# Optimization experiments

Measured on AMD Instinct MI355X. Metric: run time of the kernel, lower is better.

Reference implementation:

```python
import jax, jax.numpy as jnp
import numpy as np

B, T, HW = 2, 16, 224
S = 14            # patch size after stem: 56 // 4
FEAT = 64 * S * S # 12544 per stream


def _stem(x, w):
    # I3D truncated at MaxPool3d_2a_3x3: Conv3d 7x7x7 stride 2 (+ReLU) then MaxPool (1,3,3) stride (1,2,2)
    y = jax.lax.conv_general_dilated(x, w, window_strides=(2, 2, 2), padding='SAME',
                                     dimension_numbers=('NCDHW', 'OIDHW', 'NCDHW'))
    y = jax.nn.relu(y)
    y = jax.lax.reduce_window(y, -jnp.inf, jax.lax.max,
                              (1, 1, 1, 3, 3), (1, 1, 1, 2, 2), 'SAME')
    return y  # [B,64,8,56,56]


def _fold_and_flatten(x):
    # torch: x.unfold(3,s,s).unfold(4,s,s).permute(0,2,3,4,1,5,6).flatten(4)
    b, c, t, h, w = x.shape
    x = x.reshape(b, c, t, h // S, S, w // S, S)          # (B,C,T,hb,hi,wb,wi)
    x = x.transpose(0, 2, 3, 5, 1, 4, 6)                  # (B,T,hb,wb,C,hi,wi)
    return x.reshape(b, t, h // S, w // S, c * S * S)      # (B,8,4,4,12544)


def _fcl(fr, ff, W1, b1, W2, b2, W3, b3):
    # vectorized over (B,T,H,W); dropout inactive (eval)
    x = jnp.concatenate([fr, ff], axis=-1)                 # (B,8,4,4,25088)
    x = jax.nn.relu(jnp.einsum('bthwf,fk->bthwk', x, W1) + b1)
    x = jax.nn.relu(jnp.einsum('bthwf,fk->bthwk', x, W2) + b2)
    return jax.nn.sigmoid(jnp.einsum('bthwf,fk->bthwk', x, W3) + b3)  # (B,8,4,4,1)


def _get_mask(rgbs, flows, w_rgb, w_flow, W1, b1, W2, b2, W3, b3):
    fr = _fold_and_flatten(_stem(rgbs, w_rgb))
    ff = _fold_and_flatten(_stem(flows, w_flow))
    m = _fcl(fr, ff, W1, b1, W2, b2, W3, b3)[..., 0]       # (B,T=8,H=4,W=4)
    m = jax.image.resize(m[:, None], (m.shape[0], 1, T, HW, HW), method='trilinear')
    return m[:, 0]                                          # (B,16,224,224)


def _masking(rgbs, mask, bg):
    # rgbs*mask + bg*(1-mask), broadcast over channel dim
    return rgbs * mask[:, None] + bg[None, :, None] * (1.0 - mask[:, None])


def _feature_head(x, w_feat, Wl, bl):
    # stand-in for full frozen I3D feature backbone: stem + global pool + linear logits
    y = _stem(x, w_feat)                                    # (B,64,8,56,56)
    pooled = y.mean(axis=(2, 3, 4))                         # (B,64)
    return pooled @ Wl + bl                                 # (B,400)


def setup_inputs() -> dict:
    key = jax.random.key(0)
    ks = jax.random.split(key, 10)
    n = lambda k, s, sc=1.0: jax.random.normal(k, s, dtype=jnp.float32) * sc
    return {
        'rgbs': n(ks[0], (B, 3, T, HW, HW)),
        'flows': n(ks[1], (B, 2, T, HW, HW)),
        'img_background': n(ks[2], (3, HW, HW)),
        'w_rgb': n(ks[3], (64, 3, 7, 7, 7), 0.05),
        'w_flow': n(ks[4], (64, 2, 7, 7, 7), 0.05),
        'w_feat': n(ks[5], (64, 3, 7, 7, 7), 0.05),
        'W1': n(ks[6], (2 * FEAT, 1024), 0.01), 'b1': jnp.zeros((1024,), jnp.float32),
        'W2': n(ks[7], (1024, 256), 0.03), 'b2': jnp.zeros((256,), jnp.float32),
        'W3': n(ks[8], (256, 1), 0.06), 'b3': jnp.zeros((1,), jnp.float32),
        'Wl': n(ks[9], (64, 400), 0.1), 'bl': jnp.zeros((400,), jnp.float32),
    }


def reference(rgbs, flows, img_background, w_rgb, w_flow, w_feat,
              W1, b1, W2, b2, W3, b3, Wl, bl):
    mask = _get_mask(rgbs, flows, w_rgb, w_flow, W1, b1, W2, b2, W3, b3)
    masked0 = _masking(rgbs, mask, img_background)
    masked1 = _masking(rgbs, 1.0 - mask, img_background)
    out0 = _feature_head(masked0, w_feat, Wl, bl)
    out1 = _feature_head(masked1, w_feat, Wl, bl)
    return out0, out1, mask
```

## Files before the change

### kernel.cpp

```cpp
#include <hip/hip_runtime.h>
#include <hip/hip_bf16.h>
#include <math.h>

#define IHW 224
#define DIN 16
#define DOUT 8
#define HO 112
#define PO 56
#define DP 21
#define HP 232
#define WP 240
#define PLANE (HP * WP)

typedef __bf16 bf16x8 __attribute__((ext_vector_type(8)));
typedef float f32x4 __attribute__((ext_vector_type(4)));
typedef float f32x16 __attribute__((ext_vector_type(16)));
typedef ushort u16x8 __attribute__((ext_vector_type(8)));

__device__ __forceinline__ ushort f2bf(float f) {
  uint u = __float_as_uint(f);
  uint r = (u + 0x7FFFu + ((u >> 16) & 1u)) >> 16;
  return (ushort)r;
}
__device__ __forceinline__ float bf2f(ushort u) {
  return __uint_as_float(((uint)u) << 16);
}

__global__ void cvt_pad(const float* __restrict__ in, ushort* __restrict__ out, int nbc) {
  const int v = blockIdx.x * 256 + threadIdx.x;
  const int total = nbc * DP * HP * (WP / 2);
  if (v >= total) return;
  const int pw2 = v % (WP / 2);
  int rest = v / (WP / 2);
  const int pih = rest % HP; rest /= HP;
  const int pid = rest % DP;
  const int bc = rest / DP;
  const int id = pid - 2, ih = pih - 2;
  ushort2 o = make_ushort2(0, 0);
  if (id >= 0 && id < DIN && ih >= 0 && ih < IHW) {
    const float* src = in + ((size_t)(bc * DIN + id) * IHW + ih) * IHW;
    const int iw0 = pw2 * 2 - 2;
    if (iw0 >= 0 && iw0 < IHW) o.x = f2bf(src[iw0]);
    if (iw0 + 1 >= 0 && iw0 + 1 < IHW) o.y = f2bf(src[iw0 + 1]);
  }
  reinterpret_cast<ushort2*>(out)[v] = o;
}

__global__ void masking_pad(const float* __restrict__ rgbs, const float* __restrict__ mask,
                            const float* __restrict__ bg, ushort* __restrict__ out) {
  const int v = blockIdx.x * 256 + threadIdx.x;
  const int total = 12 * DP * HP * (WP / 2);
  if (v >= total) return;
  const int pw2 = v % (WP / 2);
  int rest = v / (WP / 2);
  const int pih = rest % HP; rest /= HP;
  const int pid = rest % DP;
  const int bc = rest / DP;
  const int head = bc / 6;
  const int r6 = bc - head * 6;
  const int b = r6 / 3, c = r6 - (r6 / 3) * 3;
  const int t = pid - 2, ih = pih - 2;
  ushort2 o = make_ushort2(0, 0);
  if (t >= 0 && t < DIN && ih >= 0 && ih < IHW) {
    const float* mrow = mask + ((size_t)(b * DIN + t)) * (IHW * IHW) + ih * IHW;
    const float* rrow = rgbs + ((size_t)((b * 3 + c) * DIN + t)) * (IHW * IHW) + ih * IHW;
    const float* brow = bg + (size_t)c * (IHW * IHW) + ih * IHW;
    const int iw0 = pw2 * 2 - 2;
#pragma unroll
    for (int j = 0; j < 2; j++) {
      const int iw = iw0 + j;
      if (iw >= 0 && iw < IHW) {
        float m = mrow[iw];
        if (head) m = 1.f - m;
        const float val = rrow[iw] * m + brow[iw] * (1.f - m);
        if (j == 0) o.x = f2bf(val); else o.y = f2bf(val);
      }
    }
  }
  reinterpret_cast<ushort2*>(out)[v] = o;
}

template<int C>
__global__ __launch_bounds__(256) void wprep(const float* __restrict__ w, ushort* __restrict__ wB) {
  constexpr int C7 = C * 7, KREAL = C * 49, KPAD = (C == 3) ? 160 : 128;
  const int idx = blockIdx.x * 256 + threadIdx.x;
  if (idx >= 64 * 7 * KPAD) return;
  const int k = idx % KPAD;
  const int rest = idx / KPAD;
  const int kw = rest % 7;
  const int oc = rest / 7;
  float val = 0.f;
  if (k < KREAL) {
    const int kd = k / C7, rem = k % C7, c = rem / 7, kh = rem % 7;
    val = w[(((oc * C + c) * 7 + kd) * 7 + kh) * 7 + kw];
  }
  wB[idx] = f2bf(val);
}

template<int C>
__global__ __launch_bounds__(256, 4) void conv_mfma(
    const ushort* __restrict__ in, const ushort* __restrict__ wB,
    ushort* __restrict__ out)
{
  constexpr int C7 = C * 7, KREAL = C * 49;
  constexpr int KPAD = (C == 3) ? 160 : 128;
  constexpr int NKS = KPAD / 16;
  constexpr int ROWB = KPAD * 2;
  constexpr int KG = KPAD / 4;
  constexpr int SROWS = 118;
  constexpr int NU2 = KG * 64 / 256;
  constexpr int BAT = NU2 / 2;

  __shared__ char smem[SROWS * ROWB];
  __shared__ int offt[KPAD];

  const int bx = blockIdx.x;
  const int hx = (bx & 7) * 28 + (bx >> 3);
  const int ho = hx >> 1, half = hx & 1;
  const int dd = blockIdx.y;
  const int bb = blockIdx.z;
  const int tid = threadIdx.x;
  const int lane = tid & 63;
  const int wv = tid >> 6;

  if (tid < KPAD) {
    const int k = (tid < KREAL) ? tid : (KREAL - 1);
    const int kd = k / C7, rem = k % C7, c = rem / 7, kh = rem % 7;
    offt[tid] = ((bb * C + c) * DP + 2 * dd + kd) * PLANE + (2 * ho + kh) * WP;
  }
  __syncthreads();

  const int piwbase = half * 112;
  for (int itb = 0; itb < 2; itb++) {
    uint v4[BAT][4];
    int sbl[BAT], sbh[BAT];
#pragma unroll
    for (int i = 0; i < BAT; i++) {
      const int id = (itb * BAT + i) * 256 + tid;
      const int kg = id >> 6, sp = id & 63;
      const int s = sp * 2;
      const bool ok = (s < SROWS);
      const int piw = piwbase + s;
      const int4 ot = *reinterpret_cast<const int4*>(&offt[kg * 4]);
      v4[i][0] = *reinterpret_cast<const uint*>(in + (size_t)(ot.x + piw));
      v4[i][1] = *reinterpret_cast<const uint*>(in + (size_t)(ot.y + piw));
      v4[i][2] = *reinterpret_cast<const uint*>(in + (size_t)(ot.z + piw));
      v4[i][3] = *reinterpret_cast<const uint*>(in + (size_t)(ot.w + piw));
      const int m = (sp & 7) << 4;
      sbl[i] = ok ? ((s * ROWB + kg * 8) ^ m) : -1;
      sbh[i] = ok ? (((s + 1) * ROWB + kg * 8) ^ m) : -1;
    }
#pragma unroll
    for (int i = 0; i < BAT; i++) {
      if (sbl[i] >= 0) {
        ushort4 lo, hi;
        lo.x = (ushort)v4[i][0]; hi.x = (ushort)(v4[i][0] >> 16);
        lo.y = (ushort)v4[i][1]; hi.y = (ushort)(v4[i][1] >> 16);
        lo.z = (ushort)v4[i][2]; hi.z = (ushort)(v4[i][2] >> 16);
        lo.w = (ushort)v4[i][3]; hi.w = (ushort)(v4[i][3] >> 16);
        *reinterpret_cast<ushort4*>(smem + sbl[i]) = lo;
        *reinterpret_cast<ushort4*>(smem + sbh[i]) = hi;
      }
    }
  }
  __syncthreads();

  const int nh = wv & 1, kseg = wv >> 1;
  const int l31 = lane & 31, khf = lane >> 5;

  int sbase[2];
#pragma unroll
  for (int mt = 0; mt < 2; mt++) {
    int wo_l = mt * 32 + l31;
    if (wo_l > 55) wo_l = 55;
    sbase[mt] = 2 * wo_l;
  }
  const ushort* wq = wB + (size_t)(nh * 32 + l31) * (7 * KPAD) + khf * 8;

  f32x16 acc[2] = {};

  if (kseg == 0) {
#pragma unroll
    for (int kw = 0; kw < 4; kw++) {
#pragma unroll
      for (int ks = 0; ks < NKS; ks++) {
        const bf16x8 b = *reinterpret_cast<const bf16x8*>(wq + kw * KPAD + ks * 16);
#pragma unroll
        for (int mt = 0; mt < 2; mt++) {
          const int s = sbase[mt] + kw;
          const int byte = (s * ROWB + ks * 32 + khf * 16) ^ (((s >> 1) & 7) << 4);
          const bf16x8 a = *reinterpret_cast<const bf16x8*>(smem + byte);
          acc[mt] = __builtin_amdgcn_mfma_f32_32x32x16_bf16(a, b, acc[mt], 0, 0, 0);
        }
      }
    }
  } else {
#pragma unroll
    for (int kw = 4; kw < 7; kw++) {
#pragma unroll
      for (int ks = 0; ks < NKS; ks++) {
        const bf16x8 b = *reinterpret_cast<const bf16x8*>(wq + kw * KPAD + ks * 16);
#pragma unroll
        for (int mt = 0; mt < 2; mt++) {
          const int s = sbase[mt] + kw;
          const int byte = (s * ROWB + ks * 32 + khf * 16) ^ (((s >> 1) & 7) << 4);
          const bf16x8 a = *reinterpret_cast<const bf16x8*>(smem + byte);
          acc[mt] = __builtin_amdgcn_mfma_f32_32x32x16_bf16(a, b, acc[mt], 0, 0, 0);
        }
      }
    }
  }

  __syncthreads();
  f32x16* red = reinterpret_cast<f32x16*>(smem);
  if (kseg == 1) {
#pragma unroll
    for (int mt = 0; mt < 2; mt++) red[(nh * 2 + mt) * 64 + lane] = acc[mt];
  }
  __syncthreads();
  if (kseg == 0) {
#pragma unroll
    for (int mt = 0; mt < 2; mt++) {
      const f32x16 p = red[(nh * 2 + mt) * 64 + lane];
#pragma unroll
      for (int r = 0; r < 16; r++) acc[mt][r] += p[r];
    }
  }
  __syncthreads();

  ushort* eLDS = reinterpret_cast<ushort*>(smem);
  if (kseg == 0) {
    const int oc = nh * 32 + l31;
#pragma unroll
    for (int mt = 0; mt < 2; mt++) {
#pragma unroll
      for (int q = 0; q < 4; q++) {
        const int wo_b = mt * 32 + q * 8 + khf * 4;
        if (wo_b < 56) {
          ushort4 r4;
          r4.x = f2bf(fmaxf(acc[mt][q * 4 + 0], 0.f));
          r4.y = f2bf(fmaxf(acc[mt][q * 4 + 1], 0.f));
          r4.z = f2bf(fmaxf(acc[mt][q * 4 + 2], 0.f));
          r4.w = f2bf(fmaxf(acc[mt][q * 4 + 3], 0.f));
          *reinterpret_cast<ushort4*>(eLDS + oc * 60 + wo_b) = r4;
        }
      }
    }
  }
  __syncthreads();
  ushort* gout = out + ((size_t)(bb * 64) * DOUT + dd) * (HO * HO) + ho * HO + half * 56;
#pragma unroll
  for (int i = 0; i < 4; i++) {
    const int idx = i * 256 + tid;
    if (idx < 896) {
      const int o2 = idx / 14;
      const int w4 = idx - o2 * 14;
      *reinterpret_cast<ushort4*>(gout + (size_t)o2 * DOUT * (HO * HO) + w4 * 4) =
          *reinterpret_cast<const ushort4*>(eLDS + o2 * 60 + w4 * 4);
    }
  }
}

__global__ void maxpool_gather(const ushort* __restrict__ in, ushort* __restrict__ X, int fbase) {
  const int idx = blockIdx.x * 256 + threadIdx.x;
  if (idx >= 2 * 64 * 8 * PO * 28) return;
  const int wo2 = idx % 28;
  const int ho = (idx / 28) % PO;
  const int rest = idx / (28 * PO);
  const ushort* p = in + (size_t)rest * (HO * HO);
  const int iwb = wo2 * 4;
  ushort m0 = 0, m1 = 0;
  for (int dh = 0; dh < 3; dh++) {
    const int ih = 2 * ho + dh;
    if (ih >= HO) break;
    const ushort* row = p + ih * HO;
    const ushort2 u0 = *reinterpret_cast<const ushort2*>(row + iwb);
    const ushort2 u1 = *reinterpret_cast<const ushort2*>(row + iwb + 2);
    const ushort e4 = (iwb + 4 < HO) ? row[iwb + 4] : (ushort)0;
    ushort a = (u0.x > u0.y) ? u0.x : u0.y;  a = (a > u1.x) ? a : u1.x;
    ushort b2 = (u1.x > u1.y) ? u1.x : u1.y; b2 = (b2 > e4) ? b2 : e4;
    m0 = (a > m0) ? a : m0;
    m1 = (b2 > m1) ? b2 : m1;
  }
  const int wo = wo2 * 2;
  const int t = rest % 8;
  const int c = (rest / 8) % 64;
  const int b = rest / 512;
  const int r = ((b * 8 + t) * 4 + ho / 14) * 4 + (wo / 14);
  const int f = fbase + c * 196 + (ho % 14) * 14 + (wo % 14);
  *reinterpret_cast<ushort2*>(X + (size_t)r * 25088 + f) = make_ushort2(m0, m1);
}

__global__ __launch_bounds__(512) void fcl1_mfma(
    const ushort* __restrict__ X, const float* __restrict__ W1, ushort* __restrict__ part)
{
  const int bn = blockIdx.x;
  const int kc = blockIdx.y;
  const int tid = threadIdx.x;
  const int lane = tid & 63;
  const int wv = tid >> 6;
  const int wm = wv >> 1, wn = wv & 1;
  const int l31 = lane & 31, kh = lane >> 5;

  __shared__ char xs[256 * 128];
  __shared__ char wsm[128 * 128];

  f32x16 acc[2][2] = {};

  const int kchunk0 = kc * 256;

  for (int kt = 0; kt < 4; kt++) {
    const int k0 = kchunk0 + kt * 64;
    __syncthreads();
#pragma unroll
    for (int i = 0; i < 4; i++) {
      const int chunk = tid + 512 * i;
      const int r = chunk >> 3, c8 = chunk & 7;
      const int4 v = *reinterpret_cast<const int4*>(X + (size_t)r * 25088 + k0 + c8 * 8);
      int byte = r * 128 + c8 * 16;
      byte ^= ((r & 7) << 4);
      *reinterpret_cast<int4*>(xs + byte) = v;
    }
    {
      const int nq = tid & 31, kp0 = tid >> 5;
#pragma unroll
      for (int h = 0; h < 2; h++) {
        const int kk = (kp0 + h * 16) * 2;
        const float4 a  = *reinterpret_cast<const float4*>(W1 + (size_t)(k0 + kk) * 1024 + bn * 128 + nq * 4);
        const float4 bq = *reinterpret_cast<const float4*>(W1 + (size_t)(k0 + kk + 1) * 1024 + bn * 128 + nq * 4);
        const float av[4] = {a.x, a.y, a.z, a.w};
        const float bv[4] = {bq.x, bq.y, bq.z, bq.w};
#pragma unroll
        for (int j = 0; j < 4; j++) {
          const int n = nq * 4 + j;
          const uint pack = (uint)f2bf(av[j]) | ((uint)f2bf(bv[j]) << 16);
          const int byte = (n * 128 + kk * 2) ^ ((n & 7) << 4);
          *reinterpret_cast<uint*>(wsm + byte) = pack;
        }
      }
    }
    __syncthreads();
#pragma unroll
    for (int ks = 0; ks < 4; ks++) {
      bf16x8 af[2], bfr[2];
#pragma unroll
      for (int m = 0; m < 2; m++) {
        const int r = wm * 64 + m * 32 + l31;
        const int byte = (r * 128 + ks * 32 + kh * 16) ^ ((r & 7) << 4);
        af[m] = *reinterpret_cast<const bf16x8*>(xs + byte);
      }
#pragma unroll
      for (int n = 0; n < 2; n++) {
        const int c = wn * 64 + n * 32 + l31;
        const int byte = (c * 128 + ks * 32 + kh * 16) ^ ((c & 7) << 4);
        bfr[n] = *reinterpret_cast<const bf16x8*>(wsm + byte);
      }
#pragma unroll
      for (int m = 0; m < 2; m++)
#pragma unroll
        for (int n = 0; n < 2; n++)
          acc[m][n] = __builtin_amdgcn_mfma_f32_32x32x16_bf16(af[m], bfr[n], acc[m][n], 0, 0, 0);
    }
  }

  ushort* pout = part + (size_t)kc * (256 * 1024);
#pragma unroll
  for (int m = 0; m < 2; m++)
#pragma unroll
    for (int n = 0; n < 2; n++)
#pragma unroll
      for (int rg = 0; rg < 16; rg++) {
        const int row = wm * 64 + m * 32 + (rg & 3) + 8 * (rg >> 2) + 4 * kh;
        const int col = bn * 128 + wn * 64 + n * 32 + l31;
        pout[(size_t)row * 1024 + col] = f2bf(acc[m][n][rg]);
      }
}

__global__ void h1_reduce(const ushort* __restrict__ part, const float* __restrict__ b1,
                          float* __restrict__ h1) {
  const int v = blockIdx.x * 256 + threadIdx.x;
  if (v >= 32768) return;
  const int r = v >> 7, n8 = v & 127;
  float s[8];
#pragma unroll
  for (int j = 0; j < 8; j++) s[j] = b1[n8 * 8 + j];
  for (int kc = 0; kc < 98; kc++) {
    const u16x8 p = *reinterpret_cast<const u16x8*>(part + (size_t)kc * 262144 + r * 1024 + n8 * 8);
#pragma unroll
    for (int j = 0; j < 8; j++) s[j] += bf2f(p[j]);
  }
#pragma unroll
  for (int j = 0; j < 8; j++) h1[r * 1024 + n8 * 8 + j] = fmaxf(s[j], 0.f);
}

__global__ __launch_bounds__(256) void fcl2_k(const float* __restrict__ h1,
                                              const float* __restrict__ W2,
                                              const float* __restrict__ b2,
                                              float* __restrict__ h2) {
  const int r0 = blockIdx.x * 4;
  const int n = threadIdx.x;
  __shared__ float xr[4][1024];
  for (int i = threadIdx.x; i < 4096; i += 256) xr[i >> 10][i & 1023] = h1[r0 * 1024 + i];
  __syncthreads();
  float acc[4] = {b2[n], b2[n], b2[n], b2[n]};
  for (int k = 0; k < 1024; k++) {
    const float w = W2[k * 256 + n];
#pragma unroll
    for (int r = 0; r < 4; r++) acc[r] += xr[r][k] * w;
  }
#pragma unroll
  for (int r = 0; r < 4; r++) h2[(r0 + r) * 256 + n] = fmaxf(acc[r], 0.f);
}

__global__ void fcl3_k(const float* __restrict__ h2, const float* __restrict__ W3,
                       const float* __restrict__ b3, float* __restrict__ ms) {
  __shared__ float w[256];
  w[threadIdx.x] = W3[threadIdx.x];
  __syncthreads();
  const int r = threadIdx.x;
  float s = b3[0];
  for (int k = 0; k < 256; k++) s += h2[r * 256 + k] * w[k];
  ms[r] = 1.f / (1.f + expf(-s));
}

__global__ void upsample_k(const float* __restrict__ ms, float* __restrict__ mask) {
  const int idx = blockIdx.x * 256 + threadIdx.x;
  if (idx >= 2 * 16 * IHW * IHW) return;
  const int w = idx % IHW;
  const int h = (idx / IHW) % IHW;
  const int t = (idx / (IHW * IHW)) % 16;
  const int b = idx / (16 * IHW * IHW);

  const float tf = t * 0.5f - 0.25f;
  const float hf = (h + 0.5f) * (1.f / 56.f) - 0.5f;
  const float wf = (w + 0.5f) * (1.f / 56.f) - 0.5f;

  int t0 = (int)floorf(tf); const float ft = tf - t0;
  int h0 = (int)floorf(hf); const float fh = hf - h0;
  int w0 = (int)floorf(wf); const float fw = wf - w0;
  const int t1 = min(t0 + 1, 7); t0 = max(t0, 0);
  const int h1 = min(h0 + 1, 3); h0 = max(h0, 0);
  const int w1 = min(w0 + 1, 3); w0 = max(w0, 0);

  const float* p = ms + b * 128;
  auto at = [&](int tt, int hh, int ww) { return p[(tt * 4 + hh) * 4 + ww]; };
  const float c00 = at(t0, h0, w0) * (1.f - fw) + at(t0, h0, w1) * fw;
  const float c01 = at(t0, h1, w0) * (1.f - fw) + at(t0, h1, w1) * fw;
  const float c10 = at(t1, h0, w0) * (1.f - fw) + at(t1, h0, w1) * fw;
  const float c11 = at(t1, h1, w0) * (1.f - fw) + at(t1, h1, w1) * fw;
  const float c0 = c00 * (1.f - fh) + c01 * fh;
  const float c1 = c10 * (1.f - fh) + c11 * fh;
  mask[idx] = c0 * (1.f - ft) + c1 * ft;
}

__global__ __launch_bounds__(256) void pool_sum_k(const ushort* __restrict__ in,
                                                  float* __restrict__ psums) {
  const int blk = blockIdx.x;
  const ushort* p = in + (size_t)blk * (HO * HO);
  float s = 0.f;
  for (int idx = threadIdx.x; idx < PO * PO; idx += 256) {
    const int ho = idx / PO, wo = idx % PO;
    ushort m = 0;
    for (int dh = 0; dh < 3; dh++) {
      const int ih = 2 * ho + dh;
      if (ih >= HO) break;
      for (int dw = 0; dw < 3; dw++) {
        const int iw = 2 * wo + dw;
        if (iw >= HO) break;
        const ushort v = p[ih * HO + iw];
        m = (v > m) ? v : m;
      }
    }
    s += bf2f(m);
  }
  __shared__ float red[256];
  red[threadIdx.x] = s;
  __syncthreads();
  for (int off = 128; off > 0; off >>= 1) {
    if (threadIdx.x < off) red[threadIdx.x] += red[threadIdx.x + off];
    __syncthreads();
  }
  if (threadIdx.x == 0) psums[blk] = red[0];
}

__global__ void logits_k(const float* __restrict__ psums, const float* __restrict__ Wl,
                         const float* __restrict__ bl, float* __restrict__ out) {
  const int idx = blockIdx.x * 256 + threadIdx.x;
  if (idx >= 1600) return;
  const int bf = idx / 400, l = idx % 400;
  float s = bl[l];
  for (int oc = 0; oc < 64; oc++) {
    float ps = 0.f;
    for (int t = 0; t < 8; t++) ps += psums[(bf * 64 + oc) * 8 + t];
    s += (ps * (1.f / 25088.f)) * Wl[oc * 400 + l];
  }
  out[idx] = s;
}

extern "C" void kernel_launch(void* const* d_in, const int* in_sizes, int n_in,
                              void* d_out, int out_size, void* d_ws, size_t ws_size,
                              hipStream_t stream) {
  const float* rgbs   = (const float*)d_in[0];
  const float* flows  = (const float*)d_in[1];
  const float* bg     = (const float*)d_in[2];
  const float* w_rgb  = (const float*)d_in[3];
  const float* w_flow = (const float*)d_in[4];
  const float* w_feat = (const float*)d_in[5];
  const float* W1     = (const float*)d_in[6];
  const float* b1     = (const float*)d_in[7];
  const float* W2     = (const float*)d_in[8];
  const float* b2     = (const float*)d_in[9];
  const float* W3     = (const float*)d_in[10];
  const float* b3     = (const float*)d_in[11];
  const float* Wl     = (const float*)d_in[12];
  const float* bl     = (const float*)d_in[13];
  float* out = (float*)d_out;

  float* ws = (float*)d_ws;
  ushort* convbuf = (ushort*)ws;
  ushort* part    = (ushort*)ws;
  ushort* X       = (ushort*)(ws + 12845056);
  ushort* rgbsP   = (ushort*)(ws + 16056320);
  ushort* flowsP  = (ushort*)(ws + 19564160);
  ushort* maskedP = (ushort*)(ws + 16056320);
  float*  h1      = ws + 23100000;
  float*  h2      = h1 + 262144;
  float*  msmall  = h2 + 65536;
  float*  psums   = msmall + 256;
  ushort* wrgb_b  = (ushort*)(psums + 2048);
  ushort* wflow_b = wrgb_b + 86016;
  ushort* wfeat_b = wflow_b + 57344;

  float* mask_full = out + 1600;

  cvt_pad<<<(3507840 + 255) / 256, 256, 0, stream>>>(rgbs, rgbsP, 6);
  cvt_pad<<<(2338560 + 255) / 256, 256, 0, stream>>>(flows, flowsP, 4);
  wprep<3><<<(64 * 7 * 160 + 255) / 256, 256, 0, stream>>>(w_rgb, wrgb_b);
  wprep<2><<<(64 * 7 * 128 + 255) / 256, 256, 0, stream>>>(w_flow, wflow_b);
  wprep<3><<<(64 * 7 * 160 + 255) / 256, 256, 0, stream>>>(w_feat, wfeat_b);

  conv_mfma<3><<<dim3(224, 8, 2), 256, 0, stream>>>(rgbsP, wrgb_b, convbuf);
  maxpool_gather<<<(1605632 + 255) / 256, 256, 0, stream>>>(convbuf, X, 0);
  conv_mfma<2><<<dim3(224, 8, 2), 256, 0, stream>>>(flowsP, wflow_b, convbuf);
  maxpool_gather<<<(1605632 + 255) / 256, 256, 0, stream>>>(convbuf, X, 12544);

  fcl1_mfma<<<dim3(8, 98), 512, 0, stream>>>(X, W1, part);
  h1_reduce<<<128, 256, 0, stream>>>(part, b1, h1);
  fcl2_k<<<64, 256, 0, stream>>>(h1, W2, b2, h2);
  fcl3_k<<<1, 256, 0, stream>>>(h2, W3, b3, msmall);
  upsample_k<<<(1605632 + 255) / 256, 256, 0, stream>>>(msmall, mask_full);

  masking_pad<<<(7015680 + 255) / 256, 256, 0, stream>>>(rgbs, mask_full, bg, maskedP);
  conv_mfma<3><<<dim3(224, 8, 4), 256, 0, stream>>>(maskedP, wfeat_b, convbuf);
  pool_sum_k<<<2048, 256, 0, stream>>>(convbuf, psums);
  logits_k<<<7, 256, 0, stream>>>(psums, Wl, bl, out);
}
```

Before: 447.5 us.

## Merge pad and weight-prep launches, fuse trilinear upsample into masking

Combines the two input convert-pad kernels into one launch and the three weight-prep kernels into one, which removes launch overhead. The masking kernel now computes the trilinear mask from the small 8x4x4 grid held in shared memory instead of reading the full-resolution mask, and handles four pixels per thread. h1_reduce is relaunched as 256 blocks of 128 threads. cvt_pad2 assumes flowsP directly follows rgbsP in the workspace, and upsample_k still writes the full mask because it is an output.

```diff
diff --git a/kernel.cpp b/kernel.cpp
--- a/kernel.cpp
+++ b/kernel.cpp
@@ -26,9 +26,10 @@
   return __uint_as_float(((uint)u) << 16);
 }
 
-__global__ void cvt_pad(const float* __restrict__ in, ushort* __restrict__ out, int nbc) {
+__global__ void cvt_pad2(const float* __restrict__ rgbs, const float* __restrict__ flows,
+                         ushort* __restrict__ out) {
   const int v = blockIdx.x * 256 + threadIdx.x;
-  const int total = nbc * DP * HP * (WP / 2);
+  const int total = 10 * DP * HP * (WP / 2);
   if (v >= total) return;
   const int pw2 = v % (WP / 2);
   int rest = v / (WP / 2);
@@ -38,7 +39,9 @@
   const int id = pid - 2, ih = pih - 2;
   ushort2 o = make_ushort2(0, 0);
   if (id >= 0 && id < DIN && ih >= 0 && ih < IHW) {
-    const float* src = in + ((size_t)(bc * DIN + id) * IHW + ih) * IHW;
+    const float* base = (bc < 6) ? (rgbs + (size_t)bc * DIN * IHW * IHW)
+                                 : (flows + (size_t)(bc - 6) * DIN * IHW * IHW);
+    const float* src = base + ((size_t)id * IHW + ih) * IHW;
     const int iw0 = pw2 * 2 - 2;
     if (iw0 >= 0 && iw0 < IHW) o.x = f2bf(src[iw0]);
     if (iw0 + 1 >= 0 && iw0 + 1 < IHW) o.y = f2bf(src[iw0 + 1]);
@@ -46,13 +49,16 @@
   reinterpret_cast<ushort2*>(out)[v] = o;
 }
 
-__global__ void masking_pad(const float* __restrict__ rgbs, const float* __restrict__ mask,
-                            const float* __restrict__ bg, ushort* __restrict__ out) {
+__global__ void masking_pad_f(const float* __restrict__ rgbs, const float* __restrict__ ms,
+                              const float* __restrict__ bg, ushort* __restrict__ out) {
+  __shared__ float ms_s[256];
+  ms_s[threadIdx.x] = ms[threadIdx.x];
+  __syncthreads();
   const int v = blockIdx.x * 256 + threadIdx.x;
-  const int total = 12 * DP * HP * (WP / 2);
+  const int total = 12 * DP * HP * (WP / 4);
   if (v >= total) return;
-  const int pw2 = v % (WP / 2);
-  int rest = v / (WP / 2);
+  const int pw4 = v % (WP / 4);
+  int rest = v / (WP / 4);
   const int pih = rest % HP; rest /= HP;
   const int pid = rest % DP;
   const int bc = rest / DP;
@@ -60,31 +66,46 @@
   const int r6 = bc - head * 6;
   const int b = r6 / 3, c = r6 - (r6 / 3) * 3;
   const int t = pid - 2, ih = pih - 2;
-  ushort2 o = make_ushort2(0, 0);
+  ushort4 o = make_ushort4(0, 0, 0, 0);
   if (t >= 0 && t < DIN && ih >= 0 && ih < IHW) {
-    const float* mrow = mask + ((size_t)(b * DIN + t)) * (IHW * IHW) + ih * IHW;
     const float* rrow = rgbs + ((size_t)((b * 3 + c) * DIN + t)) * (IHW * IHW) + ih * IHW;
     const float* brow = bg + (size_t)c * (IHW * IHW) + ih * IHW;
-    const int iw0 = pw2 * 2 - 2;
-#pragma unroll
-    for (int j = 0; j < 2; j++) {
+    const float tf = t * 0.5f - 0.25f;
+    const float hf = (ih + 0.5f) * (1.f / 56.f) - 0.5f;
+    int t0 = (int)floorf(tf); const float ft = tf - t0;
+    int h0 = (int)floorf(hf); const float fh = hf - h0;
+    const int t1 = min(t0 + 1, 7); t0 = max(t0, 0);
+    const int h1 = min(h0 + 1, 3); h0 = max(h0, 0);
+    const float* p = ms_s + b * 128;
+    const int iw0 = pw4 * 4 - 2;
+    ushort res[4] = {0, 0, 0, 0};
+#pragma unroll
+    for (int j = 0; j < 4; j++) {
       const int iw = iw0 + j;
       if (iw >= 0 && iw < IHW) {
-        float m = mrow[iw];
+        const float wf = (iw + 0.5f) * (1.f / 56.f) - 0.5f;
+        int w0 = (int)floorf(wf); const float fw = wf - w0;
+        const int w1 = min(w0 + 1, 3); w0 = max(w0, 0);
+        auto at = [&](int tt, int hh, int ww) { return p[(tt * 4 + hh) * 4 + ww]; };
+        const float c00 = at(t0, h0, w0) * (1.f - fw) + at(t0, h0, w1) * fw;
+        const float c01 = at(t0, h1, w0) * (1.f - fw) + at(t0, h1, w1) * fw;
+        const float c10 = at(t1, h0, w0) * (1.f - fw) + at(t1, h0, w1) * fw;
+        const float c11 = at(t1, h1, w0) * (1.f - fw) + at(t1, h1, w1) * fw;
+        const float c0 = c00 * (1.f - fh) + c01 * fh;
+        const float c1 = c10 * (1.f - fh) + c11 * fh;
+        float m = c0 * (1.f - ft) + c1 * ft;
         if (head) m = 1.f - m;
-        const float val = rrow[iw] * m + brow[iw] * (1.f - m);
-        if (j == 0) o.x = f2bf(val); else o.y = f2bf(val);
-      }
-    }
-  }
-  reinterpret_cast<ushort2*>(out)[v] = o;
+        res[j] = f2bf(rrow[iw] * m + brow[iw] * (1.f - m));
+      }
+    }
+    o = make_ushort4(res[0], res[1], res[2], res[3]);
+  }
+  reinterpret_cast<ushort4*>(out)[v] = o;
 }
 
 template<int C>
-__global__ __launch_bounds__(256) void wprep(const float* __restrict__ w, ushort* __restrict__ wB) {
+__device__ __forceinline__ void wprep_one(const float* __restrict__ w, ushort* __restrict__ wB, int idx) {
   constexpr int C7 = C * 7, KREAL = C * 49, KPAD = (C == 3) ? 160 : 128;
-  const int idx = blockIdx.x * 256 + threadIdx.x;
-  if (idx >= 64 * 7 * KPAD) return;
   const int k = idx % KPAD;
   const int rest = idx / KPAD;
   const int kw = rest % 7;
@@ -95,6 +116,14 @@
     val = w[(((oc * C + c) * 7 + kd) * 7 + kh) * 7 + kw];
   }
   wB[idx] = f2bf(val);
+}
+__global__ __launch_bounds__(256) void wprep_all(
+    const float* __restrict__ w_rgb, const float* __restrict__ w_flow, const float* __restrict__ w_feat,
+    ushort* __restrict__ wrgb_b, ushort* __restrict__ wflow_b, ushort* __restrict__ wfeat_b) {
+  const int idx = blockIdx.x * 256 + threadIdx.x;
+  if (idx < 71680) wprep_one<3>(w_rgb, wrgb_b, idx);
+  else if (idx < 71680 + 57344) wprep_one<2>(w_flow, wflow_b, idx - 71680);
+  else if (idx < 71680 + 57344 + 71680) wprep_one<3>(w_feat, wfeat_b, idx - 129024);
 }
 
 template<int C>
@@ -376,9 +405,10 @@
       }
 }
 
-__global__ void h1_reduce(const ushort* __restrict__ part, const float* __restrict__ b1,
-                          float* __restrict__ h1) {
-  const int v = blockIdx.x * 256 + threadIdx.x;
+__global__ __launch_bounds__(128) void h1_reduce(const ushort* __restrict__ part,
+                                                 const float* __restrict__ b1,
+                                                 float* __restrict__ h1) {
+  const int v = blockIdx.x * 128 + threadIdx.x;
   if (v >= 32768) return;
   const int r = v >> 7, n8 = v & 127;
   float s[8];
@@ -533,11 +563,9 @@
 
   float* mask_full = out + 1600;
 
-  cvt_pad<<<(3507840 + 255) / 256, 256, 0, stream>>>(rgbs, rgbsP, 6);
-  cvt_pad<<<(2338560 + 255) / 256, 256, 0, stream>>>(flows, flowsP, 4);
-  wprep<3><<<(64 * 7 * 160 + 255) / 256, 256, 0, stream>>>(w_rgb, wrgb_b);
-  wprep<2><<<(64 * 7 * 128 + 255) / 256, 256, 0, stream>>>(w_flow, wflow_b);
-  wprep<3><<<(64 * 7 * 160 + 255) / 256, 256, 0, stream>>>(w_feat, wfeat_b);
+  cvt_pad2<<<(5846400 + 255) / 256, 256, 0, stream>>>(rgbs, flows, rgbsP);
+  wprep_all<<<(200704 + 255) / 256, 256, 0, stream>>>(w_rgb, w_flow, w_feat,
+                                                      wrgb_b, wflow_b, wfeat_b);
 
   conv_mfma<3><<<dim3(224, 8, 2), 256, 0, stream>>>(rgbsP, wrgb_b, convbuf);
   maxpool_gather<<<(1605632 + 255) / 256, 256, 0, stream>>>(convbuf, X, 0);
@@ -545,12 +573,12 @@
   maxpool_gather<<<(1605632 + 255) / 256, 256, 0, stream>>>(convbuf, X, 12544);
 
   fcl1_mfma<<<dim3(8, 98), 512, 0, stream>>>(X, W1, part);
-  h1_reduce<<<128, 256, 0, stream>>>(part, b1, h1);
+  h1_reduce<<<256, 128, 0, stream>>>(part, b1, h1);
   fcl2_k<<<64, 256, 0, stream>>>(h1, W2, b2, h2);
   fcl3_k<<<1, 256, 0, stream>>>(h2, W3, b3, msmall);
   upsample_k<<<(1605632 + 255) / 256, 256, 0, stream>>>(msmall, mask_full);
 
-  masking_pad<<<(7015680 + 255) / 256, 256, 0, stream>>>(rgbs, mask_full, bg, maskedP);
+  masking_pad_f<<<(3507840 + 255) / 256, 256, 0, stream>>>(rgbs, msmall, bg, maskedP);
   conv_mfma<3><<<dim3(224, 8, 4), 256, 0, stream>>>(maskedP, wfeat_b, convbuf);
   pool_sum_k<<<2048, 256, 0, stream>>>(convbuf, psums);
   logits_k<<<7, 256, 0, stream>>>(psums, Wl, bl, out);
```

Result: no change. 441.4 us (-1.4%).
